# Kernel tuning notes

Hardware: AMD Instinct MI355X
Metric: run time of the kernel (lower is better)

## Reference

```python
import jax, jax.numpy as jnp
import numpy as np


def quat_rotate(q, v):
    # q: [..., 4] (w, x, y, z) unit quaternion; v: [..., 3]
    w = q[..., :1]
    qv = q[..., 1:]
    uv = jnp.cross(qv, v)
    uuv = jnp.cross(qv, uv)
    return v + 2.0 * (w * uv + uuv)


def setup_inputs() -> dict:
    key = jax.random.key(0)
    ks = jax.random.split(key, 5)
    B, P, S = 32, 32, 512
    shape_rlt = jax.random.uniform(ks[0], (B, P, 3), jnp.float32)        # cuboid half-dims
    trans_rlt = jax.random.normal(ks[1], (B, P, 3), jnp.float32)
    quat_rlt = jax.random.normal(ks[2], (B, P, 4), jnp.float32)
    IOUlist = jax.random.uniform(ks[3], (B, P), jnp.float32)
    coef = jax.random.uniform(ks[4], (B, P, S, 3), jnp.float32)          # interior sampling noise
    return {"shape_rlt": shape_rlt, "trans_rlt": trans_rlt,
            "quat_rlt": quat_rlt, "IOUlist": IOUlist, "coef": coef}


def reference(shape_rlt, trans_rlt, quat_rlt, IOUlist, coef):
    B, P, S, _ = coef.shape
    PS = P * S
    # normalize quaternions
    qn = quat_rlt / jnp.linalg.norm(quat_rlt, axis=-1, keepdims=True)

    # --- SamplePoint (ifSurface=False): uniform points inside each cuboid ---
    local = (2.0 * coef - 1.0) * shape_rlt[:, :, None, :]                # [B,P,S,3]
    point = quat_rotate(qn[:, :, None, :], local) + trans_rlt[:, :, None, :]
    pointRef = point.reshape(B, PS, 3)                                   # [B,P*S,3]

    # --- SamplePointWeight: per-sample weight ~ primitive volume * IOU ---
    vol = jnp.prod(shape_rlt, axis=-1) * IOUlist                         # [B,P]
    weight = jnp.repeat(vol, S, axis=1)                                  # [B,P*S]
    weight = jnp.broadcast_to(weight[:, None, :], (B, P, PS))            # expand over prims

    # --- mutex mask set1: zero out each primitive's own samples (vectorized) ---
    owner = jnp.arange(PS, dtype=jnp.int32) // S                         # [PS]
    set1 = (owner[None, :] != jnp.arange(P, dtype=jnp.int32)[:, None]).astype(coef.dtype)  # [P,PS]

    # --- partComposition_mutex: penetration TSDF of all points vs each primitive ---
    qc = qn * jnp.asarray([1.0, -1.0, -1.0, -1.0], dtype=qn.dtype)       # conjugate
    p_rel = pointRef[:, None, :, :] - trans_rlt[:, :, None, :]           # [B,P,PS,3]
    p_loc = quat_rotate(qc[:, :, None, :], p_rel)                        # into prim frame
    pen = jax.nn.relu(shape_rlt[:, :, None, :] - jnp.abs(p_loc))         # penetration depth
    tsdf = jnp.sum(pen * pen, axis=-1)                                   # [B,P,PS]
    tsdfOut = tsdf * IOUlist[:, :, None] * set1[None, :, :]
    tsdfGT = jnp.zeros_like(tsdfOut)
    return (tsdfOut, weight, tsdfGT)
```

## Files before the change

kernel.cpp:

```cpp
#include <hip/hip_runtime.h>

#define NB 32
#define NP 32
#define NS 512
#define NPS (NP * NS)

__global__ void points_kernel(const float* __restrict__ shape,
                              const float* __restrict__ trans,
                              const float* __restrict__ quat,
                              const float* __restrict__ coef,
                              float4* __restrict__ pts)
{
    int idx = blockIdx.x * blockDim.x + threadIdx.x;
    if (idx >= NB * NPS) return;
    int b = idx >> 14;
    int j = idx & (NPS - 1);
    int p = j >> 9;

    const float* q = quat + (size_t)(b * NP + p) * 4;
    float qw = q[0], qx = q[1], qy = q[2], qz = q[3];
    float inv = 1.0f / sqrtf(qw * qw + qx * qx + qy * qy + qz * qz);
    qw *= inv; qx *= inv; qy *= inv; qz *= inv;

    const float* sh = shape + (size_t)(b * NP + p) * 3;
    const float* tr = trans + (size_t)(b * NP + p) * 3;
    const float* c  = coef  + (size_t)idx * 3;

    float vx = (2.0f * c[0] - 1.0f) * sh[0];
    float vy = (2.0f * c[1] - 1.0f) * sh[1];
    float vz = (2.0f * c[2] - 1.0f) * sh[2];

    float ux = qy * vz - qz * vy;
    float uy = qz * vx - qx * vz;
    float uz = qx * vy - qy * vx;
    float uux = qy * uz - qz * uy;
    float uuy = qz * ux - qx * uz;
    float uuz = qx * uy - qy * ux;

    float px = vx + 2.0f * (qw * ux + uux) + tr[0];
    float py = vy + 2.0f * (qw * uy + uuy) + tr[1];
    float pz = vz + 2.0f * (qw * uz + uuz) + tr[2];

    pts[idx] = make_float4(px, py, pz, 0.0f);
}

__global__ void __launch_bounds__(256)
tsdf_kernel(const float* __restrict__ shape,
            const float* __restrict__ trans,
            const float* __restrict__ quat,
            const float* __restrict__ iou,
            const float4* __restrict__ pts,
            float* __restrict__ out)
{
    const size_t TOT = (size_t)NB * NP * NPS;

    int blk   = blockIdx.x;
    int chunk = blk & 15;
    int bp    = blk >> 4;
    int b     = bp >> 5;
    int p     = bp & 31;
    int j0    = chunk * 1024 + threadIdx.x * 4;

    const float* q = quat + (size_t)bp * 4;
    float qw = q[0], qx = q[1], qy = q[2], qz = q[3];
    float inv = 1.0f / sqrtf(qw * qw + qx * qx + qy * qy + qz * qz);
    qw *= inv; qx *= -inv; qy *= -inv; qz *= -inv;

    const float* sh = shape + (size_t)bp * 3;
    float sx = sh[0], sy = sh[1], sz = sh[2];
    const float* tr = trans + (size_t)bp * 3;
    float tx = tr[0], ty = tr[1], tz = tr[2];
    float iou_p = iou[bp];

    int owner = j0 >> 9;
    const float* sho = shape + (size_t)(b * NP + owner) * 3;
    float wval = sho[0] * sho[1] * sho[2] * iou[b * NP + owner];
    float mask = (owner != p) ? 1.0f : 0.0f;
    float scale = iou_p * mask;

    const float4* pbase = pts + (size_t)b * NPS + j0;

    float4 res;
    float* resv = &res.x;
    #pragma unroll
    for (int k = 0; k < 4; ++k) {
        float4 pt = pbase[k];
        float vx = pt.x - tx;
        float vy = pt.y - ty;
        float vz = pt.z - tz;
        float ux = qy * vz - qz * vy;
        float uy = qz * vx - qx * vz;
        float uz = qx * vy - qy * vx;
        float uux = qy * uz - qz * uy;
        float uuy = qz * ux - qx * uz;
        float uuz = qx * uy - qy * ux;
        float lx = vx + 2.0f * (qw * ux + uux);
        float ly = vy + 2.0f * (qw * uy + uuy);
        float lz = vz + 2.0f * (qw * uz + uuz);
        float px_ = fmaxf(sx - fabsf(lx), 0.0f);
        float py_ = fmaxf(sy - fabsf(ly), 0.0f);
        float pz_ = fmaxf(sz - fabsf(lz), 0.0f);
        float tsdf = px_ * px_ + py_ * py_ + pz_ * pz_;
        resv[k] = tsdf * scale;
    }

    size_t base = (size_t)bp * NPS + j0;
    *(float4*)(out + base)            = res;
    *(float4*)(out + TOT + base)      = make_float4(wval, wval, wval, wval);
    *(float4*)(out + 2 * TOT + base)  = make_float4(0.0f, 0.0f, 0.0f, 0.0f);
}

extern "C" void kernel_launch(void* const* d_in, const int* in_sizes, int n_in,
                              void* d_out, int out_size, void* d_ws, size_t ws_size,
                              hipStream_t stream) {
    const float* shape = (const float*)d_in[0];
    const float* trans = (const float*)d_in[1];
    const float* quat  = (const float*)d_in[2];
    const float* iou   = (const float*)d_in[3];
    const float* coef  = (const float*)d_in[4];
    float* out = (float*)d_out;
    float4* pts = (float4*)d_ws;

    int npts = NB * NPS;
    points_kernel<<<(npts + 255) / 256, 256, 0, stream>>>(shape, trans, quat, coef, pts);

    int nblocks = NB * NP * 16;
    tsdf_kernel<<<nblocks, 256, 0, stream>>>(shape, trans, quat, iou, pts, out);
}
```

Before: 43.11 us.

## Fuse point sampling into TSDF kernel and use nontemporal output stores

Removes the separate points kernel and its workspace round-trip. Each TSDF thread now recomputes the sampled world points directly from coef, loading it as three vector loads. All three output streams are written with nontemporal stores to avoid polluting cache. The cost is that each point's forward rotation is recomputed once per primitive, 32 times, and coef is reread 32 times, though from cache.

```diff
diff --git a/kernel.cpp b/kernel.cpp
--- a/kernel.cpp
+++ b/kernel.cpp
@@ -5,52 +5,15 @@
 #define NS 512
 #define NPS (NP * NS)
 
-__global__ void points_kernel(const float* __restrict__ shape,
-                              const float* __restrict__ trans,
-                              const float* __restrict__ quat,
-                              const float* __restrict__ coef,
-                              float4* __restrict__ pts)
-{
-    int idx = blockIdx.x * blockDim.x + threadIdx.x;
-    if (idx >= NB * NPS) return;
-    int b = idx >> 14;
-    int j = idx & (NPS - 1);
-    int p = j >> 9;
-
-    const float* q = quat + (size_t)(b * NP + p) * 4;
-    float qw = q[0], qx = q[1], qy = q[2], qz = q[3];
-    float inv = 1.0f / sqrtf(qw * qw + qx * qx + qy * qy + qz * qz);
-    qw *= inv; qx *= inv; qy *= inv; qz *= inv;
-
-    const float* sh = shape + (size_t)(b * NP + p) * 3;
-    const float* tr = trans + (size_t)(b * NP + p) * 3;
-    const float* c  = coef  + (size_t)idx * 3;
-
-    float vx = (2.0f * c[0] - 1.0f) * sh[0];
-    float vy = (2.0f * c[1] - 1.0f) * sh[1];
-    float vz = (2.0f * c[2] - 1.0f) * sh[2];
-
-    float ux = qy * vz - qz * vy;
-    float uy = qz * vx - qx * vz;
-    float uz = qx * vy - qy * vx;
-    float uux = qy * uz - qz * uy;
-    float uuy = qz * ux - qx * uz;
-    float uuz = qx * uy - qy * ux;
-
-    float px = vx + 2.0f * (qw * ux + uux) + tr[0];
-    float py = vy + 2.0f * (qw * uy + uuy) + tr[1];
-    float pz = vz + 2.0f * (qw * uz + uuz) + tr[2];
-
-    pts[idx] = make_float4(px, py, pz, 0.0f);
-}
+typedef float f32x4 __attribute__((ext_vector_type(4)));
 
 __global__ void __launch_bounds__(256)
-tsdf_kernel(const float* __restrict__ shape,
-            const float* __restrict__ trans,
-            const float* __restrict__ quat,
-            const float* __restrict__ iou,
-            const float4* __restrict__ pts,
-            float* __restrict__ out)
+fused_tsdf_kernel(const float* __restrict__ shape,
+                  const float* __restrict__ trans,
+                  const float* __restrict__ quat,
+                  const float* __restrict__ iou,
+                  const float* __restrict__ coef,
+                  float* __restrict__ out)
 {
     const size_t TOT = (size_t)NB * NP * NPS;
 
@@ -60,54 +23,72 @@
     int b     = bp >> 5;
     int p     = bp & 31;
     int j0    = chunk * 1024 + threadIdx.x * 4;
+    int owner = j0 >> 9;
+    int bo    = b * NP + owner;
+
+    const float* qo = quat + (size_t)bo * 4;
+    float ow = qo[0], oqx = qo[1], oqy = qo[2], oqz = qo[3];
+    float oinv = 1.0f / sqrtf(ow*ow + oqx*oqx + oqy*oqy + oqz*oqz);
+    ow *= oinv; oqx *= oinv; oqy *= oinv; oqz *= oinv;
+    const float* sho = shape + (size_t)bo * 3;
+    float osx = sho[0], osy = sho[1], osz = sho[2];
+    const float* tro = trans + (size_t)bo * 3;
+    float otx = tro[0], oty = tro[1], otz = tro[2];
+    float wval = osx * osy * osz * iou[bo];
 
     const float* q = quat + (size_t)bp * 4;
     float qw = q[0], qx = q[1], qy = q[2], qz = q[3];
-    float inv = 1.0f / sqrtf(qw * qw + qx * qx + qy * qy + qz * qz);
+    float inv = 1.0f / sqrtf(qw*qw + qx*qx + qy*qy + qz*qz);
     qw *= inv; qx *= -inv; qy *= -inv; qz *= -inv;
-
     const float* sh = shape + (size_t)bp * 3;
     float sx = sh[0], sy = sh[1], sz = sh[2];
     const float* tr = trans + (size_t)bp * 3;
     float tx = tr[0], ty = tr[1], tz = tr[2];
-    float iou_p = iou[bp];
+    float scale = iou[bp] * ((owner != p) ? 1.0f : 0.0f);
 
-    int owner = j0 >> 9;
-    const float* sho = shape + (size_t)(b * NP + owner) * 3;
-    float wval = sho[0] * sho[1] * sho[2] * iou[b * NP + owner];
-    float mask = (owner != p) ? 1.0f : 0.0f;
-    float scale = iou_p * mask;
+    const f32x4* c4 = (const f32x4*)(coef + ((size_t)bo * NS + (j0 & (NS - 1))) * 3);
+    f32x4 ca = c4[0], cb = c4[1], cc = c4[2];
+    float cf[12] = {ca.x, ca.y, ca.z, ca.w,
+                    cb.x, cb.y, cb.z, cb.w,
+                    cc.x, cc.y, cc.z, cc.w};
 
-    const float4* pbase = pts + (size_t)b * NPS + j0;
-
-    float4 res;
-    float* resv = &res.x;
+    f32x4 res;
     #pragma unroll
     for (int k = 0; k < 4; ++k) {
-        float4 pt = pbase[k];
-        float vx = pt.x - tx;
-        float vy = pt.y - ty;
-        float vz = pt.z - tz;
-        float ux = qy * vz - qz * vy;
-        float uy = qz * vx - qx * vz;
-        float uz = qx * vy - qy * vx;
-        float uux = qy * uz - qz * uy;
-        float uuy = qz * ux - qx * uz;
-        float uuz = qx * uy - qy * ux;
-        float lx = vx + 2.0f * (qw * ux + uux);
-        float ly = vy + 2.0f * (qw * uy + uuy);
-        float lz = vz + 2.0f * (qw * uz + uuz);
-        float px_ = fmaxf(sx - fabsf(lx), 0.0f);
-        float py_ = fmaxf(sy - fabsf(ly), 0.0f);
-        float pz_ = fmaxf(sz - fabsf(lz), 0.0f);
-        float tsdf = px_ * px_ + py_ * py_ + pz_ * pz_;
-        resv[k] = tsdf * scale;
+        float vx = (2.0f * cf[3*k+0] - 1.0f) * osx;
+        float vy = (2.0f * cf[3*k+1] - 1.0f) * osy;
+        float vz = (2.0f * cf[3*k+2] - 1.0f) * osz;
+        float ux = oqy*vz - oqz*vy;
+        float uy = oqz*vx - oqx*vz;
+        float uz = oqx*vy - oqy*vx;
+        float uux = oqy*uz - oqz*uy;
+        float uuy = oqz*ux - oqx*uz;
+        float uuz = oqx*uy - oqy*ux;
+        float px = vx + 2.0f*(ow*ux + uux) + otx;
+        float py = vy + 2.0f*(ow*uy + uuy) + oty;
+        float pz = vz + 2.0f*(ow*uz + uuz) + otz;
+        float rx = px - tx, ry = py - ty, rz = pz - tz;
+        float vx2 = qy*rz - qz*ry;
+        float vy2 = qz*rx - qx*rz;
+        float vz2 = qx*ry - qy*rx;
+        float wx2 = qy*vz2 - qz*vy2;
+        float wy2 = qz*vx2 - qx*vz2;
+        float wz2 = qx*vy2 - qy*vx2;
+        float lx = rx + 2.0f*(qw*vx2 + wx2);
+        float ly = ry + 2.0f*(qw*vy2 + wy2);
+        float lz = rz + 2.0f*(qw*vz2 + wz2);
+        float ppx = fmaxf(sx - fabsf(lx), 0.0f);
+        float ppy = fmaxf(sy - fabsf(ly), 0.0f);
+        float ppz = fmaxf(sz - fabsf(lz), 0.0f);
+        res[k] = (ppx*ppx + ppy*ppy + ppz*ppz) * scale;
     }
 
     size_t base = (size_t)bp * NPS + j0;
-    *(float4*)(out + base)            = res;
-    *(float4*)(out + TOT + base)      = make_float4(wval, wval, wval, wval);
-    *(float4*)(out + 2 * TOT + base)  = make_float4(0.0f, 0.0f, 0.0f, 0.0f);
+    f32x4 wv = {wval, wval, wval, wval};
+    f32x4 zv = {0.0f, 0.0f, 0.0f, 0.0f};
+    __builtin_nontemporal_store(res, (f32x4*)(out + base));
+    __builtin_nontemporal_store(wv,  (f32x4*)(out + TOT + base));
+    __builtin_nontemporal_store(zv,  (f32x4*)(out + 2 * TOT + base));
 }
 
 extern "C" void kernel_launch(void* const* d_in, const int* in_sizes, int n_in,
@@ -119,11 +100,7 @@
     const float* iou   = (const float*)d_in[3];
     const float* coef  = (const float*)d_in[4];
     float* out = (float*)d_out;
-    float4* pts = (float4*)d_ws;
-
-    int npts = NB * NPS;
-    points_kernel<<<(npts + 255) / 256, 256, 0, stream>>>(shape, trans, quat, coef, pts);
 
     int nblocks = NB * NP * 16;
-    tsdf_kernel<<<nblocks, 256, 0, stream>>>(shape, trans, quat, iou, pts, out);
+    fused_tsdf_kernel<<<nblocks, 256, 0, stream>>>(shape, trans, quat, iou, coef, out);
 }
```

Measured after the change: 48.94 us. 13.5% more time.
